# Kernel optimization log

Hardware: AMD Instinct MI355X
Metric: run time of the kernel (lower is better)

The kernel has to match this reference:

```python
import jax, jax.numpy as jnp
import numpy as np

B, CIN, COUT, H, W = 2, 256, 256, 96, 96
K, PAD, G = 3, 1, 4           # kernel, padding, deformable_groups
KK = K * K
CG = CIN // G                 # channels per deformable group


def setup_inputs() -> dict:
    key = jax.random.key(0)
    k1, k2, k3, k4 = jax.random.split(key, 4)
    feature = jax.random.normal(k1, (B, CIN, H, W), jnp.float32)
    pred_shape = jax.random.normal(k2, (B, H * W, 4), jnp.float32)
    # init_weights: normal(std=0.01), no biases
    w_offset = jax.random.normal(k3, (G * KK * 2, 4, 1, 1), jnp.float32) * 0.01
    w_deform = jax.random.normal(k4, (COUT, CIN, K, K), jnp.float32) * 0.01
    return {"feature": feature, "pred_shape": pred_shape,
            "w_offset": w_offset, "w_deform": w_deform}


def reference(feature, pred_shape, w_offset, w_deform):
    # pred_shape: (B, H*W, 4) -> (B, 4, H, W); detached in the original
    ps = jnp.transpose(pred_shape, (0, 2, 1)).reshape(B, -1, H, W)
    ps = jax.lax.stop_gradient(ps)
    # 1x1 offset conv: (B, G*2*KK, H, W)
    offset = jnp.einsum('bchw,oc->bohw', ps, w_offset[:, :, 0, 0])
    # mmcv layout per group: [y_k0, x_k0, y_k1, x_k1, ...]
    off = offset.reshape(B, G, KK, 2, H, W)
    off_y, off_x = off[:, :, :, 0], off[:, :, :, 1]   # (B, G, KK, H, W)

    kk = jnp.arange(KK)
    ky = (kk // K).reshape(KK, 1, 1).astype(jnp.float32)
    kx = (kk % K).reshape(KK, 1, 1).astype(jnp.float32)
    yy = jnp.arange(H, dtype=jnp.float32).reshape(1, H, 1)
    xx = jnp.arange(W, dtype=jnp.float32).reshape(1, 1, W)
    # sampling positions (stride=1, dilation=1): (B, G, KK, H, W)
    py = (yy - PAD + ky)[None, None] + off_y
    px = (xx - PAD + kx)[None, None] + off_x

    img = feature.reshape(B, G, CG, H * W)

    def gather(yi, xi):
        # zero outside the image (matches DCN bilinear with zero padding)
        valid = ((yi >= 0) & (yi < H) & (xi >= 0) & (xi < W)).astype(feature.dtype)
        idx = jnp.clip(yi, 0, H - 1) * W + jnp.clip(xi, 0, W - 1)
        v = jnp.take_along_axis(img, idx.reshape(B, G, 1, KK * H * W), axis=3)
        return v.reshape(B, G, CG, KK, H, W) * valid[:, :, None]

    y0 = jnp.floor(py); x0 = jnp.floor(px)
    ly = py - y0; lx = px - x0
    y0i = y0.astype(jnp.int32); x0i = x0.astype(jnp.int32)

    val = ((1 - ly) * (1 - lx))[:, :, None] * gather(y0i, x0i) \
        + ((1 - ly) * lx)[:, :, None] * gather(y0i, x0i + 1) \
        + (ly * (1 - lx))[:, :, None] * gather(y0i + 1, x0i) \
        + (ly * lx)[:, :, None] * gather(y0i + 1, x0i + 1)

    sampled = val.reshape(B, CIN, KK, H, W)
    out = jnp.einsum('bckhw,ock->bohw', sampled, w_deform.reshape(COUT, CIN, KK))
    return jax.nn.relu(out)
```

## Files before the change

### kernel.cpp

```cpp
#include <hip/hip_runtime.h>
#include <hip/hip_bf16.h>
#include <stdint.h>

#define HH   96
#define WW   96
#define HW   9216
#define CIN  256
#define COUT 256
#define NB   2
#define NG   4
#define CG   64
#define KK   9
#define KTOT 2304
#define KB   288
#define TS   8
#define WIN  12
#define SCH  32

typedef __attribute__((ext_vector_type(8))) short short8;
typedef __attribute__((ext_vector_type(4))) float f32x4;
typedef __attribute__((ext_vector_type(4))) uint32_t u32x4;

__device__ __forceinline__ uint32_t pk2bf(float v0, float v1) {
    __hip_bfloat162 h = __float22bfloat162_rn(make_float2(v0, v1));
    uint32_t u;
    __builtin_memcpy(&u, &h, 4);
    return u;
}

__global__ __launch_bounds__(256) void prep_A(const float* __restrict__ wd,
                                              uint16_t* __restrict__ Ablk) {
    int t  = blockIdx.x * 256 + threadIdx.x;
    int kb = t % KB;
    int o  = t / KB;
    int kkA = kb >> 5;
    int c0A = (kb & 31) * 8;
    const float* src = wd + (size_t)o * KTOT + c0A * KK + kkA;
    float a[8];
#pragma unroll
    for (int e = 0; e < 8; ++e) a[e] = src[e * KK];
    uint16_t* dst = Ablk + ((size_t)kb * 256 + o) * 8;
    u32x4 v;
    v.x = pk2bf(a[0], a[1]);
    v.y = pk2bf(a[2], a[3]);
    v.z = pk2bf(a[4], a[5]);
    v.w = pk2bf(a[6], a[7]);
    *(u32x4*)dst = v;
}

__global__ __launch_bounds__(256) void sampler(const float* __restrict__ feature,
                                               const float* __restrict__ pred,
                                               const float* __restrict__ woff,
                                               uint16_t* __restrict__ S) {
    __shared__ float ft[SCH * WIN * WIN];

    int tid = threadIdx.x;
    int cb = blockIdx.y, b = blockIdx.z;
    int ch0 = cb * SCH;
    int g = ch0 >> 6;
    int ty = blockIdx.x / (WW / TS), tx = blockIdx.x % (WW / TS);
    int r0 = ty * TS, c0 = tx * TS;
    int rlo = min(max(r0 - 2, 0), HH - WIN);
    int clo = min(max(c0 - 2, 0), WW - WIN);

    const float* fg = feature + ((size_t)(b * CIN + ch0)) * HW;
    for (int e = tid; e < SCH * WIN * WIN; e += 256) {
        int ch = e / (WIN * WIN);
        int re = e - ch * (WIN * WIN);
        int rr = re / WIN, cc = re - rr * WIN;
        ft[e] = fg[(size_t)ch * HW + (rlo + rr) * WW + clo + cc];
    }
    __syncthreads();

    int lane = tid & 63, wv = tid >> 6;
    int lr = lane >> 3, lc = lane & 7;
    int hy = r0 + lr, hx = c0 + lc;
    int p = hy * WW + hx;
    float4 ps4 = *(const float4*)(pred + ((size_t)b * HW + p) * 4);

    const float* ftw = ft + (wv * 8) * (WIN * WIN);
    const float* fgw = fg + (size_t)(wv * 8) * HW;
    int kb_base = cb * 4 + wv;

#pragma unroll
    for (int kk = 0; kk < KK; ++kk) {
        const float* wy = woff + (g * KK + kk) * 8;
        float offy = ps4.x * wy[0] + ps4.y * wy[1] + ps4.z * wy[2] + ps4.w * wy[3];
        float offx = ps4.x * wy[4] + ps4.y * wy[5] + ps4.z * wy[6] + ps4.w * wy[7];
        float py = (float)(hy - 1 + kk / 3) + offy;
        float px = (float)(hx - 1 + kk % 3) + offx;
        float fy = floorf(py), fx = floorf(px);
        int y0 = (int)fy, x0 = (int)fx;
        float ly = py - fy, lx = px - fx;
        int r = min(max(y0, 0), HH - 2);
        int q = min(max(x0, 0), WW - 2);
        float wyA = (y0 == r) ? (1.f - ly) : ((y0 == -1) ? ly : 0.f);
        float wyB = (y0 == r) ? ly : ((y0 == HH - 1) ? (1.f - ly) : 0.f);
        float wxA = (x0 == q) ? (1.f - lx) : ((x0 == -1) ? lx : 0.f);
        float wxB = (x0 == q) ? lx : ((x0 == WW - 1) ? (1.f - lx) : 0.f);
        float c00 = wyA * wxA, c01 = wyA * wxB;
        float c10 = wyB * wxA, c11 = wyB * wxB;

        bool fast = (r >= rlo) & (r <= rlo + WIN - 2) &
                    (q >= clo) & (q <= clo + WIN - 2);

        uint16_t* Sp = S + (((size_t)b * KB + (kk * 32 + kb_base)) * HW + p) * 8;
        uint32_t pk[4];

        if (fast) {
            int base = (r - rlo) * WIN + (q - clo);
#pragma unroll
            for (int ep = 0; ep < 4; ++ep) {
                const float* f0 = ftw + (2 * ep) * (WIN * WIN) + base;
                const float* f1 = f0 + (WIN * WIN);
                float v0 = c00 * f0[0] + c01 * f0[1] + c10 * f0[WIN] + c11 * f0[WIN + 1];
                float v1 = c00 * f1[0] + c01 * f1[1] + c10 * f1[WIN] + c11 * f1[WIN + 1];
                pk[ep] = pk2bf(v0, v1);
            }
        } else {
            size_t gb = (size_t)r * WW + q;
#pragma unroll
            for (int ep = 0; ep < 4; ++ep) {
                const float* f0 = fgw + (size_t)(2 * ep) * HW + gb;
                const float* f1 = f0 + HW;
                float v0 = c00 * f0[0] + c01 * f0[1] + c10 * f0[WW] + c11 * f0[WW + 1];
                float v1 = c00 * f1[0] + c01 * f1[1] + c10 * f1[WW] + c11 * f1[WW + 1];
                pk[ep] = pk2bf(v0, v1);
            }
        }
        u32x4 vv = {pk[0], pk[1], pk[2], pk[3]};
        *(u32x4*)(Sp) = vv;
    }
}

__global__ __launch_bounds__(64, 2) void gemm_kernel(const uint16_t* __restrict__ S,
                                                     const uint16_t* __restrict__ Ablk,
                                                     float* __restrict__ out) {
    int lane = threadIdx.x;
    int bid = blockIdx.x;
    int xcd = bid & 7;
    int j   = bid >> 3;
    int my  = j & 3;
    int pairid = xcd * 36 + (j >> 2);
    int b  = pairid / 144;
    int py = pairid % 144;
    int o0 = my * 64, col0 = py * 64;
    int kc = lane >> 4, il = lane & 15;

    const uint16_t* Ap = Ablk + ((size_t)kc * 256 + o0 + il) * 8;
    const uint16_t* Bp = S + (size_t)b * KB * HW * 8 + ((size_t)kc * HW + col0 + il) * 8;
    const size_t Astep = (size_t)4 * 256 * 8;
    const size_t Bstep = (size_t)4 * HW * 8;

    f32x4 acc[4][4];
#pragma unroll
    for (int m = 0; m < 4; ++m)
#pragma unroll
        for (int n = 0; n < 4; ++n) acc[m][n] = (f32x4){0.f, 0.f, 0.f, 0.f};

    const int NT = KTOT / 32;

    short8 a0[4], b0[4], a1[4], b1[4];

#define LOADT(t, areg, breg)                                                   \
    {                                                                          \
        const uint16_t* ap = Ap + (size_t)(t) * Astep;                         \
        const uint16_t* bp = Bp + (size_t)(t) * Bstep;                         \
        areg[0] = *(const short8*)(ap + 0 * 16 * 8);                           \
        areg[1] = *(const short8*)(ap + 1 * 16 * 8);                           \
        areg[2] = *(const short8*)(ap + 2 * 16 * 8);                           \
        areg[3] = *(const short8*)(ap + 3 * 16 * 8);                           \
        breg[0] = *(const short8*)(bp + 0 * 16 * 8);                           \
        breg[1] = *(const short8*)(bp + 1 * 16 * 8);                           \
        breg[2] = *(const short8*)(bp + 2 * 16 * 8);                           \
        breg[3] = *(const short8*)(bp + 3 * 16 * 8);                           \
    }

#define MFMAT(areg, breg)                                                      \
    {                                                                          \
        _Pragma("unroll")                                                      \
        for (int m = 0; m < 4; ++m)                                            \
            _Pragma("unroll")                                                  \
            for (int n = 0; n < 4; ++n)                                        \
                acc[m][n] = __builtin_amdgcn_mfma_f32_16x16x32_bf16(           \
                    areg[m], breg[n], acc[m][n], 0, 0, 0);                     \
    }

    LOADT(0, a0, b0);
    LOADT(1, a1, b1);

    for (int tt = 0; tt < NT; tt += 2) {
        MFMAT(a0, b0);
        if (tt + 2 < NT) LOADT(tt + 2, a0, b0);
        MFMAT(a1, b1);
        if (tt + 3 < NT) LOADT(tt + 3, a1, b1);
    }
#undef LOADT
#undef MFMAT

    int r4 = kc * 4;
    size_t obase = ((size_t)b * COUT + o0) * HW + col0;
#pragma unroll
    for (int m = 0; m < 4; ++m)
#pragma unroll
        for (int n = 0; n < 4; ++n)
#pragma unroll
            for (int r = 0; r < 4; ++r) {
                float v = acc[m][n][r];
                v = v > 0.f ? v : 0.f;
                out[obase + (size_t)(m * 16 + r4 + r) * HW + n * 16 + il] = v;
            }
}

extern "C" void kernel_launch(void* const* d_in, const int* in_sizes, int n_in,
                              void* d_out, int out_size, void* d_ws, size_t ws_size,
                              hipStream_t stream) {
    (void)in_sizes; (void)n_in; (void)out_size; (void)ws_size;
    const float* feature = (const float*)d_in[0];
    const float* pred    = (const float*)d_in[1];
    const float* woff    = (const float*)d_in[2];
    const float* wdef    = (const float*)d_in[3];
    float* out = (float*)d_out;

    const size_t S_BYTES = (size_t)NB * KB * HW * 8 * 2;
    uint16_t* S    = (uint16_t*)d_ws;
    uint16_t* Ablk = (uint16_t*)((char*)d_ws + S_BYTES);

    hipLaunchKernelGGL(prep_A, dim3(288), dim3(256), 0, stream, wdef, Ablk);
    hipLaunchKernelGGL(sampler, dim3((HH / TS) * (WW / TS), CIN / SCH, NB), dim3(256), 0, stream,
                       feature, pred, woff, S);
    hipLaunchKernelGGL(gemm_kernel, dim3(8 * (HW / 64) * NB / 8 * 4), dim3(64), 0, stream,
                       S, Ablk, out);
}
```

Baseline: 77.12 us.

## Precompute bilinear weight tables, pair channels in LDS, halve GEMM column tile

Adds a kernel that computes the per-group sampling corner weights (packed as fp16) and window/global base indices once, so the sampler no longer repeats the offset and bilinear math for every channel block. The sampler now stores channel pairs interleaved as float2 in LDS, with a padded row width of 13, to cut LDS load instructions and bank conflicts. The GEMM tile shrinks from 64 to 32 columns and the grid doubles for more parallelism. In exchange it adds an extra launch and a table write/read through memory, and fp16 weights lose some precision.

```diff
diff --git a/kernel.cpp b/kernel.cpp
--- a/kernel.cpp
+++ b/kernel.cpp
@@ -1,5 +1,6 @@
 #include <hip/hip_runtime.h>
 #include <hip/hip_bf16.h>
+#include <hip/hip_fp16.h>
 #include <stdint.h>
 
 #define HH   96
@@ -15,6 +16,7 @@
 #define KB   288
 #define TS   8
 #define WIN  12
+#define W2   13
 #define SCH  32
 
 typedef __attribute__((ext_vector_type(8))) short short8;
@@ -26,6 +28,19 @@
     uint32_t u;
     __builtin_memcpy(&u, &h, 4);
     return u;
+}
+
+__device__ __forceinline__ uint32_t pkhalf(float a, float b) {
+    __half2 h = __halves2half2(__float2half(a), __float2half(b));
+    uint32_t u;
+    __builtin_memcpy(&u, &h, 4);
+    return u;
+}
+
+__device__ __forceinline__ float2 unpkhalf(uint32_t u) {
+    __half2 h;
+    __builtin_memcpy(&h, &u, 4);
+    return __half22float2(h);
 }
 
 __global__ __launch_bounds__(256) void prep_A(const float* __restrict__ wd,
@@ -48,11 +63,52 @@
     *(u32x4*)dst = v;
 }
 
+__global__ __launch_bounds__(256) void wtab(const float* __restrict__ pred,
+                                            const float* __restrict__ woff,
+                                            u32x4* __restrict__ T) {
+    int idx = blockIdx.x * 256 + threadIdx.x;
+    int p   = idx % HW;
+    int rem = idx / HW;
+    int kk  = rem % 9;
+    int gg  = (rem / 9) % NG;
+    int b   = rem / (9 * NG);
+    int hy = p / WW, hx = p % WW;
+    int r0 = (hy >> 3) * TS, c0 = (hx >> 3) * TS;
+    int rlo = min(max(r0 - 2, 0), HH - WIN);
+    int clo = min(max(c0 - 2, 0), WW - WIN);
+
+    float4 ps4 = *(const float4*)(pred + ((size_t)b * HW + p) * 4);
+    const float* wy = woff + (gg * KK + kk) * 8;
+    float offy = ps4.x * wy[0] + ps4.y * wy[1] + ps4.z * wy[2] + ps4.w * wy[3];
+    float offx = ps4.x * wy[4] + ps4.y * wy[5] + ps4.z * wy[6] + ps4.w * wy[7];
+    float py = (float)(hy - 1 + kk / 3) + offy;
+    float px = (float)(hx - 1 + kk % 3) + offx;
+    float fy = floorf(py), fx = floorf(px);
+    int y0 = (int)fy, x0 = (int)fx;
+    float ly = py - fy, lx = px - fx;
+    int r = min(max(y0, 0), HH - 2);
+    int q = min(max(x0, 0), WW - 2);
+    float wyA = (y0 == r) ? (1.f - ly) : ((y0 == -1) ? ly : 0.f);
+    float wyB = (y0 == r) ? ly : ((y0 == HH - 1) ? (1.f - ly) : 0.f);
+    float wxA = (x0 == q) ? (1.f - lx) : ((x0 == -1) ? lx : 0.f);
+    float wxB = (x0 == q) ? lx : ((x0 == WW - 1) ? (1.f - lx) : 0.f);
+    bool fast = (r >= rlo) & (r <= rlo + WIN - 2) &
+                (q >= clo) & (q <= clo + WIN - 2);
+    uint32_t fb = fast ? (uint32_t)((r - rlo) * W2 + (q - clo)) : 0xFFFFu;
+    uint32_t gb = (uint32_t)(r * WW + q);
+
+    u32x4 e;
+    e.x = pkhalf(wyA * wxA, wyA * wxB);
+    e.y = pkhalf(wyB * wxA, wyB * wxB);
+    e.z = fb | (gb << 16);
+    e.w = 0;
+    T[idx] = e;
+}
+
 __global__ __launch_bounds__(256) void sampler(const float* __restrict__ feature,
-                                               const float* __restrict__ pred,
-                                               const float* __restrict__ woff,
+                                               const u32x4* __restrict__ T,
                                                uint16_t* __restrict__ S) {
-    __shared__ float ft[SCH * WIN * WIN];
+    __shared__ float2 ft2[(SCH / 2) * WIN * W2];
 
     int tid = threadIdx.x;
     int cb = blockIdx.y, b = blockIdx.z;
@@ -63,62 +119,52 @@
     int rlo = min(max(r0 - 2, 0), HH - WIN);
     int clo = min(max(c0 - 2, 0), WW - WIN);
 
+    float* ftf = (float*)ft2;
     const float* fg = feature + ((size_t)(b * CIN + ch0)) * HW;
     for (int e = tid; e < SCH * WIN * WIN; e += 256) {
         int ch = e / (WIN * WIN);
         int re = e - ch * (WIN * WIN);
         int rr = re / WIN, cc = re - rr * WIN;
-        ft[e] = fg[(size_t)ch * HW + (rlo + rr) * WW + clo + cc];
+        ftf[(ch >> 1) * (WIN * W2 * 2) + (rr * W2 + cc) * 2 + (ch & 1)] =
+            fg[(size_t)ch * HW + (rlo + rr) * WW + clo + cc];
     }
     __syncthreads();
 
     int lane = tid & 63, wv = tid >> 6;
     int lr = lane >> 3, lc = lane & 7;
-    int hy = r0 + lr, hx = c0 + lc;
-    int p = hy * WW + hx;
-    float4 ps4 = *(const float4*)(pred + ((size_t)b * HW + p) * 4);
-
-    const float* ftw = ft + (wv * 8) * (WIN * WIN);
+    int p = (r0 + lr) * WW + c0 + lc;
+
+    const float2* ftw = ft2 + (wv * 4) * (WIN * W2);
     const float* fgw = fg + (size_t)(wv * 8) * HW;
     int kb_base = cb * 4 + wv;
+    const u32x4* Tg = T + ((size_t)(b * NG + g) * KK) * HW + p;
 
 #pragma unroll
     for (int kk = 0; kk < KK; ++kk) {
-        const float* wy = woff + (g * KK + kk) * 8;
-        float offy = ps4.x * wy[0] + ps4.y * wy[1] + ps4.z * wy[2] + ps4.w * wy[3];
-        float offx = ps4.x * wy[4] + ps4.y * wy[5] + ps4.z * wy[6] + ps4.w * wy[7];
-        float py = (float)(hy - 1 + kk / 3) + offy;
-        float px = (float)(hx - 1 + kk % 3) + offx;
-        float fy = floorf(py), fx = floorf(px);
-        int y0 = (int)fy, x0 = (int)fx;
-        float ly = py - fy, lx = px - fx;
-        int r = min(max(y0, 0), HH - 2);
-        int q = min(max(x0, 0), WW - 2);
-        float wyA = (y0 == r) ? (1.f - ly) : ((y0 == -1) ? ly : 0.f);
-        float wyB = (y0 == r) ? ly : ((y0 == HH - 1) ? (1.f - ly) : 0.f);
-        float wxA = (x0 == q) ? (1.f - lx) : ((x0 == -1) ? lx : 0.f);
-        float wxB = (x0 == q) ? lx : ((x0 == WW - 1) ? (1.f - lx) : 0.f);
-        float c00 = wyA * wxA, c01 = wyA * wxB;
-        float c10 = wyB * wxA, c11 = wyB * wxB;
-
-        bool fast = (r >= rlo) & (r <= rlo + WIN - 2) &
-                    (q >= clo) & (q <= clo + WIN - 2);
+        u32x4 e = Tg[(size_t)kk * HW];
+        uint32_t ex = e.x, ey = e.y, ez = e.z;
+        float2 w01 = unpkhalf(ex);
+        float2 w23 = unpkhalf(ey);
+        float c00 = w01.x, c01 = w01.y, c10 = w23.x, c11 = w23.y;
+        uint32_t fb = ez & 0xFFFFu;
+        uint32_t gbi = ez >> 16;
 
         uint16_t* Sp = S + (((size_t)b * KB + (kk * 32 + kb_base)) * HW + p) * 8;
         uint32_t pk[4];
 
-        if (fast) {
-            int base = (r - rlo) * WIN + (q - clo);
+        if (fb != 0xFFFFu) {
+            int base = (int)fb;
 #pragma unroll
             for (int ep = 0; ep < 4; ++ep) {
-                const float* f0 = ftw + (2 * ep) * (WIN * WIN) + base;
-                const float* f1 = f0 + (WIN * WIN);
-                float v0 = c00 * f0[0] + c01 * f0[1] + c10 * f0[WIN] + c11 * f0[WIN + 1];
-                float v1 = c00 * f1[0] + c01 * f1[1] + c10 * f1[WIN] + c11 * f1[WIN + 1];
+                const float2* f0 = ftw + ep * (WIN * W2) + base;
+                float2 p00 = f0[0], p01 = f0[1];
+                float2 p10 = f0[W2], p11 = f0[W2 + 1];
+                float v0 = c00 * p00.x + c01 * p01.x + c10 * p10.x + c11 * p11.x;
+                float v1 = c00 * p00.y + c01 * p01.y + c10 * p10.y + c11 * p11.y;
                 pk[ep] = pk2bf(v0, v1);
             }
         } else {
-            size_t gb = (size_t)r * WW + q;
+            size_t gb = (size_t)gbi;
 #pragma unroll
             for (int ep = 0; ep < 4; ++ep) {
                 const float* f0 = fgw + (size_t)(2 * ep) * HW + gb;
@@ -141,10 +187,10 @@
     int xcd = bid & 7;
     int j   = bid >> 3;
     int my  = j & 3;
-    int pairid = xcd * 36 + (j >> 2);
-    int b  = pairid / 144;
-    int py = pairid % 144;
-    int o0 = my * 64, col0 = py * 64;
+    int pairid = xcd * 72 + (j >> 2);
+    int b  = pairid / 288;
+    int pc = pairid % 288;
+    int o0 = my * 64, col0 = pc * 32;
     int kc = lane >> 4, il = lane & 15;
 
     const uint16_t* Ap = Ablk + ((size_t)kc * 256 + o0 + il) * 8;
@@ -152,15 +198,15 @@
     const size_t Astep = (size_t)4 * 256 * 8;
     const size_t Bstep = (size_t)4 * HW * 8;
 
-    f32x4 acc[4][4];
+    f32x4 acc[4][2];
 #pragma unroll
     for (int m = 0; m < 4; ++m)
 #pragma unroll
-        for (int n = 0; n < 4; ++n) acc[m][n] = (f32x4){0.f, 0.f, 0.f, 0.f};
+        for (int n = 0; n < 2; ++n) acc[m][n] = (f32x4){0.f, 0.f, 0.f, 0.f};
 
     const int NT = KTOT / 32;
 
-    short8 a0[4], b0[4], a1[4], b1[4];
+    short8 a0[4], b0[2], a1[4], b1[2];
 
 #define LOADT(t, areg, breg)                                                   \
     {                                                                          \
@@ -172,8 +218,6 @@
         areg[3] = *(const short8*)(ap + 3 * 16 * 8);                           \
         breg[0] = *(const short8*)(bp + 0 * 16 * 8);                           \
         breg[1] = *(const short8*)(bp + 1 * 16 * 8);                           \
-        breg[2] = *(const short8*)(bp + 2 * 16 * 8);                           \
-        breg[3] = *(const short8*)(bp + 3 * 16 * 8);                           \
     }
 
 #define MFMAT(areg, breg)                                                      \
@@ -181,7 +225,7 @@
         _Pragma("unroll")                                                      \
         for (int m = 0; m < 4; ++m)                                            \
             _Pragma("unroll")                                                  \
-            for (int n = 0; n < 4; ++n)                                        \
+            for (int n = 0; n < 2; ++n)                                        \
                 acc[m][n] = __builtin_amdgcn_mfma_f32_16x16x32_bf16(           \
                     areg[m], breg[n], acc[m][n], 0, 0, 0);                     \
     }
@@ -203,7 +247,7 @@
 #pragma unroll
     for (int m = 0; m < 4; ++m)
 #pragma unroll
-        for (int n = 0; n < 4; ++n)
+        for (int n = 0; n < 2; ++n)
 #pragma unroll
             for (int r = 0; r < 4; ++r) {
                 float v = acc[m][n][r];
@@ -223,12 +267,16 @@
     float* out = (float*)d_out;
 
     const size_t S_BYTES = (size_t)NB * KB * HW * 8 * 2;
+    const size_t A_BYTES = (size_t)KB * 256 * 8 * 2;
     uint16_t* S    = (uint16_t*)d_ws;
     uint16_t* Ablk = (uint16_t*)((char*)d_ws + S_BYTES);
+    u32x4*    T    = (u32x4*)((char*)d_ws + S_BYTES + A_BYTES);
 
     hipLaunchKernelGGL(prep_A, dim3(288), dim3(256), 0, stream, wdef, Ablk);
+    hipLaunchKernelGGL(wtab, dim3((NB * NG * KK * HW) / 256), dim3(256), 0, stream,
+                       pred, woff, T);
     hipLaunchKernelGGL(sampler, dim3((HH / TS) * (WW / TS), CIN / SCH, NB), dim3(256), 0, stream,
-                       feature, pred, woff, S);
-    hipLaunchKernelGGL(gemm_kernel, dim3(8 * (HW / 64) * NB / 8 * 4), dim3(64), 0, stream,
+                       feature, T, S);
+    hipLaunchKernelGGL(gemm_kernel, dim3(2304), dim3(64), 0, stream,
                        S, Ablk, out);
 }
```

After: 94.94 us. +23.1%, slower.
